# Optimization experiments

Hardware: AMD Instinct MI355X
Metric: run time of the kernel (lower is better)

The kernel has to match this reference:

```python
import jax, jax.numpy as jnp
import numpy as np

KS = 3      # kernel_size
PAD = 1     # padding
STRIDE = 1
B, C_IN, C_OUT, H, W = 4, 64, 128, 128, 128


def _conv(x, w, stride, padding):
    return jax.lax.conv_general_dilated(
        x, w, (stride, stride), padding,
        dimension_numbers=("NCHW", "OIHW", "NCHW"))


def setup_inputs() -> dict:
    key = jax.random.key(0)
    k1, k2, k3, k4 = jax.random.split(key, 4)
    N = KS * KS
    x = jax.random.normal(k1, (B, C_IN, H, W), jnp.float32)
    # offset conv: Conv2d(inc, 2*ks*ks, 3, padding=1, stride=1). (Original inits
    # weight to 0; we use small random weights so the bilinear gather is exercised.)
    w_off = jax.random.normal(k2, (2 * N, C_IN, 3, 3), jnp.float32) * 0.01
    b_off = jax.random.normal(k3, (2 * N,), jnp.float32) * 0.01
    # main conv: Conv2d(inc, outc, ks, stride=ks, bias=False)
    w_conv = jax.random.normal(k4, (C_OUT, C_IN, KS, KS), jnp.float32) / np.sqrt(C_IN * KS * KS)
    return {"x": x, "w_off": w_off, "b_off": b_off, "w_conv": w_conv}


def deform_forward(x, w_off, b_off, w_conv):
    ks, pad, stride = KS, PAD, STRIDE
    N = ks * ks
    offset = _conv(x, w_off, stride, [(1, 1), (1, 1)]) + b_off[None, :, None, None]
    b, _, h, w = offset.shape
    xp = jnp.pad(x, ((0, 0), (0, 0), (pad, pad), (pad, pad)))
    Hp, Wp = xp.shape[2], xp.shape[3]

    # p_n: relative kernel offsets, layout [y coords (N), x coords (N)]
    r = jnp.arange(-(ks - 1) // 2, (ks - 1) // 2 + 1)
    pny, pnx = jnp.meshgrid(r, r, indexing="ij")
    p_n = jnp.concatenate([pny.ravel(), pnx.ravel()]).astype(offset.dtype).reshape(1, 2 * N, 1, 1)

    # p_0: absolute output-pixel centers (1-based due to zero padding)
    p0y, p0x = jnp.meshgrid(jnp.arange(1, h * stride + 1, stride),
                            jnp.arange(1, w * stride + 1, stride), indexing="ij")
    p_0 = jnp.concatenate([jnp.tile(p0y[None, None], (1, N, 1, 1)),
                           jnp.tile(p0x[None, None], (1, N, 1, 1))], axis=1).astype(offset.dtype)

    p = (p_0 + p_n + offset).transpose(0, 2, 3, 1)  # (b, h, w, 2N)

    # four integer corners (indices are non-differentiable / detached)
    q_lt_f = jnp.floor(jax.lax.stop_gradient(p))
    q_rb_f = q_lt_f + 1

    def clamp_yx(q):
        return jnp.concatenate([jnp.clip(q[..., :N], 0, Hp - 1),
                                jnp.clip(q[..., N:], 0, Wp - 1)], axis=-1).astype(jnp.int32)

    q_lt = clamp_yx(q_lt_f)
    q_rb = clamp_yx(q_rb_f)
    q_lb = jnp.concatenate([q_lt[..., :N], q_rb[..., N:]], axis=-1)
    q_rt = jnp.concatenate([q_rb[..., :N], q_lt[..., N:]], axis=-1)

    # points falling in the padding region snap to floor(p)
    mask = jnp.concatenate([
        (p[..., :N] < pad) | (p[..., :N] > Hp - 1 - pad),
        (p[..., N:] < pad) | (p[..., N:] > Wp - 1 - pad)], axis=-1).astype(p.dtype)
    mask = jax.lax.stop_gradient(mask)
    floor_p = jnp.floor(p)
    p = p * (1 - mask) + floor_p * mask
    p = jnp.concatenate([jnp.clip(p[..., :N], 0, Hp - 1),
                         jnp.clip(p[..., N:], 0, Wp - 1)], axis=-1)

    f = lambda q: q.astype(p.dtype)
    g_lt = (1 + (f(q_lt[..., :N]) - p[..., :N])) * (1 + (f(q_lt[..., N:]) - p[..., N:]))
    g_rb = (1 - (f(q_rb[..., :N]) - p[..., :N])) * (1 - (f(q_rb[..., N:]) - p[..., N:]))
    g_lb = (1 + (f(q_lb[..., :N]) - p[..., :N])) * (1 - (f(q_lb[..., N:]) - p[..., N:]))
    g_rt = (1 - (f(q_rt[..., :N]) - p[..., :N])) * (1 + (f(q_rt[..., N:]) - p[..., N:]))

    c = xp.shape[1]
    x_flat = xp.reshape(b, c, Hp * Wp)  # (b, c, Hp*Wp)

    def get_x_q(q):
        idx = (q[..., :N] * Wp + q[..., N:]).reshape(b, 1, h * w * N)
        return jnp.take_along_axis(x_flat, idx, axis=2).reshape(b, c, h, w, N)

    x_off = (g_lt[:, None] * get_x_q(q_lt) + g_rb[:, None] * get_x_q(q_rb)
             + g_lb[:, None] * get_x_q(q_lb) + g_rt[:, None] * get_x_q(q_rt))

    # (b, c, h, w, N=ks*ks) -> (b, c, h*ks, w*ks): sample n maps to kernel cell (n//ks, n%ks)
    x_off = x_off.reshape(b, c, h, w, ks, ks).transpose(0, 1, 2, 4, 3, 5).reshape(b, c, h * ks, w * ks)

    return _conv(x_off, w_conv, ks, "VALID")  # stride=ks, no bias


def reference(x, w_off, b_off, w_conv):
    return deform_forward(x, w_off, b_off, w_conv)
```

## Files before the change

kernel.cpp:

```cpp
#include <hip/hip_runtime.h>
#include <hip/hip_fp16.h>

#define NB 4
#define CI 64
#define CO 128
#define HH 128
#define WW 128
#define HWSZ (HH*WW)
#define TOTPX (NB*HWSZ)
#define NN 9

using half8 = __attribute__((ext_vector_type(8))) _Float16;
using f32x4 = __attribute__((ext_vector_type(4))) float;
using f32x2 = __attribute__((ext_vector_type(2))) float;

__global__ __launch_bounds__(256) void k_prep_w(const float* __restrict__ w,
                                                unsigned short* __restrict__ waF,
                                                const float* __restrict__ w_off,
                                                float* __restrict__ wP) {
    int t = blockIdx.x * 256 + threadIdx.x;
    if (t < CO * 576) {
        int oc = t / 576, r = t - oc * 576;
        int c = r / 9, n = r - c * 9;
        int i = oc >> 4, col = oc & 15;
        int ks = c >> 5, koct = (c >> 3) & 3, e = c & 7;
        int lane = koct * 16 + col;
        waF[(n * 16 + i * 2 + ks) * 512 + lane * 8 + e] =
            __half_as_ushort(__float2half_rn(w[t]));
    }
    if (t < 18 * 576) {
        int oc = t / 576, r = t - oc * 576;
        wP[r * 20 + oc] = w_off[t];
    }
}

__global__ __launch_bounds__(512, 8) void k_offsets(
    const float* __restrict__ x, const float* __restrict__ wP,
    const float* __restrict__ b_off, uchar4* __restrict__ dC,
    ushort4* __restrict__ dG, unsigned short* __restrict__ xT)
{
    __shared__ f32x2 sm[512 * 9];
    int bid = blockIdx.x;
    int b = bid >> 8, rem = bid & 255, y = rem >> 1, x0 = (rem & 1) << 6;
    int t = threadIdx.x;
    int pxl = t & 63;
    int g   = __builtin_amdgcn_readfirstlane(t >> 6);
    int xg = x0 + pxl;

    f32x2 a2[9];
    #pragma unroll
    for (int i = 0; i < 9; i++) a2[i] = {0.f, 0.f};

    #pragma unroll 2
    for (int ci = 0; ci < 8; ci++) {
        int cg = g * 8 + ci;
        const float* xpl = x + (size_t)(b * CI + cg) * HWSZ;
        #pragma unroll
        for (int ky = 0; ky < 3; ky++) {
            int yy = y + ky - 1;
            if ((unsigned)yy >= 128u) continue;
            const float* xr = xpl + yy * WW;
            #pragma unroll
            for (int kx = 0; kx < 3; kx++) {
                int xx = xg + kx - 1;
                float v = ((unsigned)xx < 128u) ? xr[xx] : 0.f;
                const f32x2* wr2 = (const f32x2*)(wP + (cg * 9 + ky * 3 + kx) * 20);
                f32x2 v2 = {v, v};
                #pragma unroll
                for (int j = 0; j < 9; j++)
                    a2[j] = __builtin_elementwise_fma(v2, wr2[j], a2[j]);
            }
        }
    }

    {
        const float* xc = x + ((size_t)(b * CI + g * 8) * HH + y) * WW + xg;
        unsigned short c8[8];
        #pragma unroll
        for (int ci = 0; ci < 8; ci++)
            c8[ci] = __half_as_ushort(__float2half_rn(xc[(size_t)ci * HWSZ]));
        size_t pbase = (size_t)((b * HH + y) * WW + xg) * 64 + g * 8;
        *(uint4*)(xT + pbase) = *(const uint4*)&c8[0];
    }

    #pragma unroll
    for (int i = 0; i < 9; i++) sm[t * 9 + i] = a2[i];
    __syncthreads();

    for (int task = t; task < 576; task += 512) {
        int p2 = task & 63, n = task >> 6;
        float ay = b_off[n], ax = b_off[9 + n];
        int jy = n >> 1, cy = n & 1;
        int jx = (9 + n) >> 1, cx = (9 + n) & 1;
        #pragma unroll
        for (int gg = 0; gg < 8; gg++) {
            ay += sm[(gg * 64 + p2) * 9 + jy][cy];
            ax += sm[(gg * 64 + p2) * 9 + jx][cx];
        }
        float py  = (float)(y + (n / 3)) + ay;
        float pxc = (float)(x0 + p2 + (n % 3)) + ax;
        float fy = floorf(py), fx = floorf(pxc);
        if (py  < 1.f || py  > 128.f) py  = fy;
        if (pxc < 1.f || pxc > 128.f) pxc = fx;
        py  = fminf(fmaxf(py,  0.f), 129.f);
        pxc = fminf(fmaxf(pxc, 0.f), 129.f);

        fy = floorf(py); fx = floorf(pxc);
        int y0 = (int)fy, x0i = (int)fx;
        int y1 = min(y0 + 1, 129), x1 = min(x0i + 1, 129);
        float wyl = 1.f + (fy - py);
        float wyr = 1.f - ((float)y1 - py);
        float wxl = 1.f + (fx - pxc);
        float wxr = 1.f - ((float)x1 - pxc);
        float glt = wyl * wxl, grb = wyr * wxr, glb = wyl * wxr, grt = wyr * wxl;
        if ((unsigned)(y0  - 1) >= 128u) { glt = 0.f; glb = 0.f; }
        if ((unsigned)(y1  - 1) >= 128u) { grb = 0.f; grt = 0.f; }
        if ((unsigned)(x0i - 1) >= 128u) { glt = 0.f; grt = 0.f; }
        if ((unsigned)(x1  - 1) >= 128u) { grb = 0.f; glb = 0.f; }

        uchar4 cu;
        cu.x = (unsigned char)min(max(y0  - 1, 0), 127);
        cu.y = (unsigned char)min(max(y1  - 1, 0), 127);
        cu.z = (unsigned char)min(max(x0i - 1, 0), 127);
        cu.w = (unsigned char)min(max(x1  - 1, 0), 127);
        ushort4 gu;
        gu.x = __half_as_ushort(__float2half_rn(glt));
        gu.y = __half_as_ushort(__float2half_rn(grb));
        gu.z = __half_as_ushort(__float2half_rn(glb));
        gu.w = __half_as_ushort(__float2half_rn(grt));
        int pixIdx = (b * HH + y) * WW + x0 + p2;
        dC[n * TOTPX + pixIdx] = cu;
        dG[n * TOTPX + pixIdx] = gu;
    }
}

__global__ __launch_bounds__(256, 2) void k_main(
    const unsigned short* __restrict__ xT, const unsigned short* __restrict__ waF,
    const uchar4* __restrict__ dC, const ushort4* __restrict__ dG,
    float* __restrict__ out)
{
    __shared__ __align__(16) unsigned short Wl[2][8192];
    __shared__ __align__(16) unsigned short Rd[4][2][1024];

    int bid0 = blockIdx.x;
    int bid  = ((bid0 & 7) << 6) | (bid0 >> 3);
    int b = bid >> 7, y = bid & 127;

    int t = threadIdx.x, lane = t & 63, wv = t >> 6;
    int col = lane & 15, koct = lane >> 4;
    int gp = lane >> 2, gq = lane & 3;
    int qo = gq * 8;
    int rowbase = (b * HH + y) * WW;
    int pixG0 = rowbase + wv * 32 + gp;
    int pixG1 = pixG0 + 16;
    const unsigned short* xb = xT + (size_t)b * (HWSZ * 64);

    half8 raw0[8], raw1[8];
    f32x4 acc0[8], acc1[8];
    #pragma unroll
    for (int i = 0; i < 8; i++) { acc0[i] = {0.f,0.f,0.f,0.f}; acc1[i] = {0.f,0.f,0.f,0.f}; }

    auto stage = [&](int kc, int buf) {
        #pragma unroll
        for (int p = 0; p < 4; p++) {
            const unsigned short* gsrc = waF + kc * 8192 + wv * 512 + p * 2048 + lane * 8;
            __builtin_amdgcn_global_load_lds(
                (const __attribute__((address_space(1))) unsigned int*)gsrc,
                (__attribute__((address_space(3))) unsigned int*)&Wl[buf][wv * 512 + p * 2048],
                16, 0, 0);
        }
    };
    auto issue = [&](uchar4 cu, half8* raw) {
        int o00 = (((int)cu.x * WW) + (int)cu.z) << 6;
        int o11 = (((int)cu.y * WW) + (int)cu.w) << 6;
        int o01 = (((int)cu.x * WW) + (int)cu.w) << 6;
        int o10 = (((int)cu.y * WW) + (int)cu.z) << 6;
        raw[0] = *(const half8*)(xb + o00 + qo);
        raw[1] = *(const half8*)(xb + o11 + qo);
        raw[2] = *(const half8*)(xb + o01 + qo);
        raw[3] = *(const half8*)(xb + o10 + qo);
        raw[4] = *(const half8*)(xb + o00 + qo + 32);
        raw[5] = *(const half8*)(xb + o11 + qo + 32);
        raw[6] = *(const half8*)(xb + o01 + qo + 32);
        raw[7] = *(const half8*)(xb + o10 + qo + 32);
    };
    auto combine_store = [&](const half8* raw, ushort4 gu, unsigned short* rbase) {
        __half2 q0 = __half2half2(__ushort_as_half(gu.x));
        __half2 q1 = __half2half2(__ushort_as_half(gu.y));
        __half2 q2 = __half2half2(__ushort_as_half(gu.z));
        __half2 q3 = __half2half2(__ushort_as_half(gu.w));
        #pragma unroll
        for (int ks = 0; ks < 2; ks++) {
            __half2 vm[4];
            #pragma unroll
            for (int m = 0; m < 4; m++) {
                __half2 v = __hmul2(((const __half2*)&raw[ks * 4 + 0])[m], q0);
                v = __hfma2(((const __half2*)&raw[ks * 4 + 1])[m], q1, v);
                v = __hfma2(((const __half2*)&raw[ks * 4 + 2])[m], q2, v);
                v = __hfma2(((const __half2*)&raw[ks * 4 + 3])[m], q3, v);
                vm[m] = v;
            }
            int gz = (4 * ks + gq) ^ (gp & 7);
            *(uint4*)(rbase + gp * 64 + gz * 8) = *(const uint4*)vm;
        }
    };

    stage(0, 0);
    __builtin_amdgcn_sched_barrier(0);
    uchar4 cuA0 = dC[pixG0],         cuA1 = dC[pixG1];
    ushort4 guA0 = dG[pixG0],        guA1 = dG[pixG1];
    uchar4 cuB0 = dC[TOTPX + pixG0], cuB1 = dC[TOTPX + pixG1];
    ushort4 guB0 = dG[TOTPX + pixG0], guB1 = dG[TOTPX + pixG1];
    __builtin_amdgcn_sched_barrier(0);
    issue(cuA0, raw0);
    issue(cuA1, raw1);
    __builtin_amdgcn_sched_barrier(0);
    asm volatile("s_waitcnt vmcnt(24)" ::: "memory");
    __builtin_amdgcn_s_barrier();
    __builtin_amdgcn_sched_barrier(0);

#define ITER(KC)                                                              \
  {                                                                           \
    if ((KC) < 8) stage((KC) + 1, ((KC) & 1) ^ 1);                            \
    __builtin_amdgcn_sched_barrier(0);                                        \
    uchar4 cuN0, cuN1; ushort4 guN0, guN1;                                    \
    if ((KC) < 7) {                                                           \
      cuN0 = dC[((KC)+2) * TOTPX + pixG0]; guN0 = dG[((KC)+2) * TOTPX + pixG0]; \
      cuN1 = dC[((KC)+2) * TOTPX + pixG1]; guN1 = dG[((KC)+2) * TOTPX + pixG1]; \
    }                                                                         \
    __builtin_amdgcn_sched_barrier(0);                                        \
    combine_store(raw0, guA0, &Rd[wv][0][0]);                                 \
    combine_store(raw1, guA1, &Rd[wv][1][0]);                                 \
    asm volatile("s_waitcnt lgkmcnt(0)" ::: "memory");                        \
    __builtin_amdgcn_sched_barrier(0);                                        \
    half8 bfr0[2], bfr1[2];                                                   \
    _Pragma("unroll")                                                         \
    for (int ks = 0; ks < 2; ks++) {                                          \
      int gz = (4 * ks + koct) ^ (col & 7);                                   \
      bfr0[ks] = *(const half8*)(&Rd[wv][0][0] + col * 64 + gz * 8);          \
      bfr1[ks] = *(const half8*)(&Rd[wv][1][0] + col * 64 + gz * 8);          \
    }                                                                         \
    __builtin_amdgcn_sched_barrier(0);                                        \
    if ((KC) < 8) { issue(cuB0, raw0); issue(cuB1, raw1); }                   \
    __builtin_amdgcn_sched_barrier(0);                                        \
    __builtin_amdgcn_s_setprio(1);                                            \
    { const unsigned short* wl = &Wl[(KC) & 1][0];                            \
      _Pragma("unroll")                                                       \
      for (int ks = 0; ks < 2; ks++)                                          \
        _Pragma("unroll")                                                     \
        for (int i = 0; i < 8; i++) {                                         \
          half8 af = *(const half8*)(wl + (i * 2 + ks) * 512 + lane * 8);     \
          acc0[i] = __builtin_amdgcn_mfma_f32_16x16x32_f16(af, bfr0[ks],      \
                                                           acc0[i], 0, 0, 0); \
          acc1[i] = __builtin_amdgcn_mfma_f32_16x16x32_f16(af, bfr1[ks],      \
                                                           acc1[i], 0, 0, 0); \
        } }                                                                   \
    __builtin_amdgcn_s_setprio(0);                                            \
    if ((KC) < 8) {                                                           \
      if ((KC) < 7) asm volatile("s_waitcnt vmcnt(20)" ::: "memory");         \
      else          asm volatile("s_waitcnt vmcnt(16)" ::: "memory");         \
      __builtin_amdgcn_s_barrier();                                           \
      __builtin_amdgcn_sched_barrier(0);                                      \
    }                                                                         \
    guA0 = guB0; guA1 = guB1;                                                 \
    cuB0 = ((KC) < 7) ? cuN0 : cuB0; guB0 = ((KC) < 7) ? guN0 : guB0;         \
    cuB1 = ((KC) < 7) ? cuN1 : cuB1; guB1 = ((KC) < 7) ? guN1 : guB1;         \
  }

    ITER(0) ITER(1) ITER(2) ITER(3) ITER(4) ITER(5) ITER(6) ITER(7) ITER(8)
#undef ITER

    int ob0 = b * CO * HWSZ + y * WW + wv * 32 + col;
    #pragma unroll
    for (int i = 0; i < 8; i++)
        #pragma unroll
        for (int r = 0; r < 4; r++) {
            int oc = i * 16 + koct * 4 + r;
            out[ob0 + oc * HWSZ]      = acc0[i][r];
            out[ob0 + oc * HWSZ + 16] = acc1[i][r];
        }
}

extern "C" void kernel_launch(void* const* d_in, const int* in_sizes, int n_in,
                              void* d_out, int out_size, void* d_ws, size_t ws_size,
                              hipStream_t stream) {
    const float* x      = (const float*)d_in[0];
    const float* w_off  = (const float*)d_in[1];
    const float* b_off  = (const float*)d_in[2];
    const float* w_conv = (const float*)d_in[3];
    float* out = (float*)d_out;

    char* wsb = (char*)d_ws;
    unsigned short* xT  = (unsigned short*)wsb;
    uchar4*         dC  = (uchar4*)(wsb + (size_t)TOTPX * 64 * 2);
    ushort4*        dG  = (ushort4*)(wsb + (size_t)TOTPX * 64 * 2 + (size_t)NN * TOTPX * 4);
    unsigned short* waF = (unsigned short*)(wsb + (size_t)TOTPX * 64 * 2
                                            + (size_t)NN * TOTPX * 4 + (size_t)NN * TOTPX * 8);
    float*          wP  = (float*)(wsb + (size_t)TOTPX * 64 * 2
                                   + (size_t)NN * TOTPX * 4 + (size_t)NN * TOTPX * 8
                                   + (size_t)CO * 576 * 2);

    k_prep_w<<<(CO * 576 + 255) / 256, 256, 0, stream>>>(w_conv, waF, w_off, wP);
    k_offsets<<<1024, 512, 0, stream>>>(x, wP, b_off, dC, dG, xT);
    k_main<<<512, 256, 0, stream>>>(xT, waF, dC, dG, out);
}
```

Baseline: 57.39 us.

## Halve per-block pixel tile in k_main to raise occupancy and block count

```diff
diff --git a/kernel.cpp b/kernel.cpp
--- a/kernel.cpp
+++ b/kernel.cpp
@@ -134,31 +134,29 @@
     }
 }
 
-__global__ __launch_bounds__(256, 2) void k_main(
+__global__ __launch_bounds__(256, 4) void k_main(
     const unsigned short* __restrict__ xT, const unsigned short* __restrict__ waF,
     const uchar4* __restrict__ dC, const ushort4* __restrict__ dG,
     float* __restrict__ out)
 {
     __shared__ __align__(16) unsigned short Wl[2][8192];
-    __shared__ __align__(16) unsigned short Rd[4][2][1024];
+    __shared__ __align__(16) unsigned short Rd[4][1024];
 
     int bid0 = blockIdx.x;
-    int bid  = ((bid0 & 7) << 6) | (bid0 >> 3);
-    int b = bid >> 7, y = bid & 127;
+    int bid  = ((bid0 & 7) << 7) | (bid0 >> 3);
+    int b = bid >> 8, rem = bid & 255, y = rem >> 1, x0 = (rem & 1) << 6;
 
     int t = threadIdx.x, lane = t & 63, wv = t >> 6;
     int col = lane & 15, koct = lane >> 4;
     int gp = lane >> 2, gq = lane & 3;
     int qo = gq * 8;
-    int rowbase = (b * HH + y) * WW;
-    int pixG0 = rowbase + wv * 32 + gp;
-    int pixG1 = pixG0 + 16;
+    int pixG = (b * HH + y) * WW + x0 + wv * 16 + gp;
     const unsigned short* xb = xT + (size_t)b * (HWSZ * 64);
 
-    half8 raw0[8], raw1[8];
-    f32x4 acc0[8], acc1[8];
-    #pragma unroll
-    for (int i = 0; i < 8; i++) { acc0[i] = {0.f,0.f,0.f,0.f}; acc1[i] = {0.f,0.f,0.f,0.f}; }
+    half8 raw[8];
+    f32x4 acc[8];
+    #pragma unroll
+    for (int i = 0; i < 8; i++) acc[i] = {0.f, 0.f, 0.f, 0.f};
 
     auto stage = [&](int kc, int buf) {
         #pragma unroll
@@ -170,7 +168,7 @@
                 16, 0, 0);
         }
     };
-    auto issue = [&](uchar4 cu, half8* raw) {
+    auto issue = [&](uchar4 cu) {
         int o00 = (((int)cu.x * WW) + (int)cu.z) << 6;
         int o11 = (((int)cu.y * WW) + (int)cu.w) << 6;
         int o01 = (((int)cu.x * WW) + (int)cu.w) << 6;
@@ -184,7 +182,7 @@
         raw[6] = *(const half8*)(xb + o01 + qo + 32);
         raw[7] = *(const half8*)(xb + o10 + qo + 32);
     };
-    auto combine_store = [&](const half8* raw, ushort4 gu, unsigned short* rbase) {
+    auto combine_store = [&](ushort4 gu) {
         __half2 q0 = __half2half2(__ushort_as_half(gu.x));
         __half2 q1 = __half2half2(__ushort_as_half(gu.y));
         __half2 q2 = __half2half2(__ushort_as_half(gu.z));
@@ -201,21 +199,18 @@
                 vm[m] = v;
             }
             int gz = (4 * ks + gq) ^ (gp & 7);
-            *(uint4*)(rbase + gp * 64 + gz * 8) = *(const uint4*)vm;
+            *(uint4*)(&Rd[wv][0] + gp * 64 + gz * 8) = *(const uint4*)vm;
         }
     };
 
     stage(0, 0);
     __builtin_amdgcn_sched_barrier(0);
-    uchar4 cuA0 = dC[pixG0],         cuA1 = dC[pixG1];
-    ushort4 guA0 = dG[pixG0],        guA1 = dG[pixG1];
-    uchar4 cuB0 = dC[TOTPX + pixG0], cuB1 = dC[TOTPX + pixG1];
-    ushort4 guB0 = dG[TOTPX + pixG0], guB1 = dG[TOTPX + pixG1];
-    __builtin_amdgcn_sched_barrier(0);
-    issue(cuA0, raw0);
-    issue(cuA1, raw1);
-    __builtin_amdgcn_sched_barrier(0);
-    asm volatile("s_waitcnt vmcnt(24)" ::: "memory");
+    uchar4  cuA = dC[pixG];          ushort4 guA = dG[pixG];
+    uchar4  cuB = dC[TOTPX + pixG];  ushort4 guB = dG[TOTPX + pixG];
+    __builtin_amdgcn_sched_barrier(0);
+    issue(cuA);
+    __builtin_amdgcn_sched_barrier(0);
+    asm volatile("s_waitcnt vmcnt(8)" ::: "memory");
     __builtin_amdgcn_s_barrier();
     __builtin_amdgcn_sched_barrier(0);
 
@@ -223,25 +218,21 @@
   {                                                                           \
     if ((KC) < 8) stage((KC) + 1, ((KC) & 1) ^ 1);                            \
     __builtin_amdgcn_sched_barrier(0);                                        \
-    uchar4 cuN0, cuN1; ushort4 guN0, guN1;                                    \
-    if ((KC) < 7) {                                                           \
-      cuN0 = dC[((KC)+2) * TOTPX + pixG0]; guN0 = dG[((KC)+2) * TOTPX + pixG0]; \
-      cuN1 = dC[((KC)+2) * TOTPX + pixG1]; guN1 = dG[((KC)+2) * TOTPX + pixG1]; \
-    }                                                                         \
-    __builtin_amdgcn_sched_barrier(0);                                        \
-    combine_store(raw0, guA0, &Rd[wv][0][0]);                                 \
-    combine_store(raw1, guA1, &Rd[wv][1][0]);                                 \
+    uchar4 cuN; ushort4 guN;                                                  \
+    if ((KC) < 7) { cuN = dC[((KC)+2) * TOTPX + pixG];                        \
+                    guN = dG[((KC)+2) * TOTPX + pixG]; }                      \
+    __builtin_amdgcn_sched_barrier(0);                                        \
+    combine_store(guA);                                                       \
     asm volatile("s_waitcnt lgkmcnt(0)" ::: "memory");                        \
     __builtin_amdgcn_sched_barrier(0);                                        \
-    half8 bfr0[2], bfr1[2];                                                   \
+    half8 bfr[2];                                                             \
     _Pragma("unroll")                                                         \
     for (int ks = 0; ks < 2; ks++) {                                          \
       int gz = (4 * ks + koct) ^ (col & 7);                                   \
-      bfr0[ks] = *(const half8*)(&Rd[wv][0][0] + col * 64 + gz * 8);          \
-      bfr1[ks] = *(const half8*)(&Rd[wv][1][0] + col * 64 + gz * 8);          \
+      bfr[ks] = *(const half8*)(&Rd[wv][0] + col * 64 + gz * 8);              \
     }                                                                         \
     __builtin_amdgcn_sched_barrier(0);                                        \
-    if ((KC) < 8) { issue(cuB0, raw0); issue(cuB1, raw1); }                   \
+    if ((KC) < 8) issue(cuB);                                                 \
     __builtin_amdgcn_sched_barrier(0);                                        \
     __builtin_amdgcn_s_setprio(1);                                            \
     { const unsigned short* wl = &Wl[(KC) & 1][0];                            \
@@ -250,34 +241,29 @@
         _Pragma("unroll")                                                     \
         for (int i = 0; i < 8; i++) {                                         \
           half8 af = *(const half8*)(wl + (i * 2 + ks) * 512 + lane * 8);     \
-          acc0[i] = __builtin_amdgcn_mfma_f32_16x16x32_f16(af, bfr0[ks],      \
-                                                           acc0[i], 0, 0, 0); \
-          acc1[i] = __builtin_amdgcn_mfma_f32_16x16x32_f16(af, bfr1[ks],      \
-                                                           acc1[i], 0, 0, 0); \
-        } }                                                                   \
+          acc[i] = __builtin_amdgcn_mfma_f32_16x16x32_f16(af, bfr[ks],        \
+                                                          acc[i], 0, 0, 0); } } \
     __builtin_amdgcn_s_setprio(0);                                            \
     if ((KC) < 8) {                                                           \
-      if ((KC) < 7) asm volatile("s_waitcnt vmcnt(20)" ::: "memory");         \
-      else          asm volatile("s_waitcnt vmcnt(16)" ::: "memory");         \
+      if ((KC) < 7) asm volatile("s_waitcnt vmcnt(10)" ::: "memory");         \
+      else          asm volatile("s_waitcnt vmcnt(8)"  ::: "memory");         \
       __builtin_amdgcn_s_barrier();                                           \
       __builtin_amdgcn_sched_barrier(0);                                      \
     }                                                                         \
-    guA0 = guB0; guA1 = guB1;                                                 \
-    cuB0 = ((KC) < 7) ? cuN0 : cuB0; guB0 = ((KC) < 7) ? guN0 : guB0;         \
-    cuB1 = ((KC) < 7) ? cuN1 : cuB1; guB1 = ((KC) < 7) ? guN1 : guB1;         \
+    cuA = cuB; guA = guB;                                                     \
+    cuB = ((KC) < 7) ? cuN : cuB; guB = ((KC) < 7) ? guN : guB;               \
   }
 
     ITER(0) ITER(1) ITER(2) ITER(3) ITER(4) ITER(5) ITER(6) ITER(7) ITER(8)
 #undef ITER
 
-    int ob0 = b * CO * HWSZ + y * WW + wv * 32 + col;
+    int ob0 = b * CO * HWSZ + y * WW + x0 + wv * 16 + col;
     #pragma unroll
     for (int i = 0; i < 8; i++)
         #pragma unroll
         for (int r = 0; r < 4; r++) {
             int oc = i * 16 + koct * 4 + r;
-            out[ob0 + oc * HWSZ]      = acc0[i][r];
-            out[ob0 + oc * HWSZ + 16] = acc1[i][r];
+            out[ob0 + oc * HWSZ] = acc[i][r];
         }
 }
 
@@ -302,5 +288,5 @@
 
     k_prep_w<<<(CO * 576 + 255) / 256, 256, 0, stream>>>(w_conv, waF, w_off, wP);
     k_offsets<<<1024, 512, 0, stream>>>(x, wP, b_off, dC, dG, xT);
-    k_main<<<512, 256, 0, stream>>>(xT, waF, dC, dG, out);
-}
+    k_main<<<1024, 256, 0, stream>>>(xT, waF, dC, dG, out);
+}
```

Result: no change. 58.39 us (+1.7%).

## Compute two adjacent pixels per thread in offset conv with float2 loads

Applied to the files above, without the earlier changes.

```diff
diff --git a/kernel.cpp b/kernel.cpp
--- a/kernel.cpp
+++ b/kernel.cpp
@@ -34,24 +34,24 @@
     }
 }
 
-__global__ __launch_bounds__(512, 8) void k_offsets(
+__global__ __launch_bounds__(512, 4) void k_offsets(
     const float* __restrict__ x, const float* __restrict__ wP,
     const float* __restrict__ b_off, uchar4* __restrict__ dC,
     ushort4* __restrict__ dG, unsigned short* __restrict__ xT)
 {
-    __shared__ f32x2 sm[512 * 9];
+    __shared__ f32x2 sm[4 * 128 * 9];
     int bid = blockIdx.x;
-    int b = bid >> 8, rem = bid & 255, y = rem >> 1, x0 = (rem & 1) << 6;
+    int b = bid >> 7, y = bid & 127;
     int t = threadIdx.x;
-    int pxl = t & 63;
-    int g   = __builtin_amdgcn_readfirstlane(t >> 6);
-    int xg = x0 + pxl;
-
-    f32x2 a2[9];
-    #pragma unroll
-    for (int i = 0; i < 9; i++) a2[i] = {0.f, 0.f};
-
-    #pragma unroll 2
+    int pr = t & 63;
+    int g  = __builtin_amdgcn_readfirstlane(t >> 6);
+
+    f32x2 a0[9], a1[9];
+    #pragma unroll
+    for (int i = 0; i < 9; i++) { a0[i] = {0.f, 0.f}; a1[i] = {0.f, 0.f}; }
+    unsigned short c16a[8], c16b[8];
+
+    #pragma unroll
     for (int ci = 0; ci < 8; ci++) {
         int cg = g * 8 + ci;
         const float* xpl = x + (size_t)(b * CI + cg) * HWSZ;
@@ -59,78 +59,117 @@
         for (int ky = 0; ky < 3; ky++) {
             int yy = y + ky - 1;
             if ((unsigned)yy >= 128u) continue;
-            const float* xr = xpl + yy * WW;
+            const float* xr = xpl + yy * WW + 2 * pr;
+            int offL = (pr > 0)  ? -2 : 0;
+            int offR = (pr < 63) ?  2 : 0;
+            f32x2 v0 = *(const f32x2*)(xr);
+            f32x2 vl = *(const f32x2*)(xr + offL);
+            f32x2 vr = *(const f32x2*)(xr + offR);
+            if (pr == 0)  vl = (f32x2){0.f, 0.f};
+            if (pr == 63) vr = (f32x2){0.f, 0.f};
+            if (ky == 1) {
+                c16a[ci] = __half_as_ushort(__float2half_rn(v0[0]));
+                c16b[ci] = __half_as_ushort(__float2half_rn(v0[1]));
+            }
             #pragma unroll
             for (int kx = 0; kx < 3; kx++) {
-                int xx = xg + kx - 1;
-                float v = ((unsigned)xx < 128u) ? xr[xx] : 0.f;
+                float ta = (kx == 0) ? vl[1] : (kx == 1) ? v0[0] : v0[1];
+                float tb = (kx == 0) ? v0[0] : (kx == 1) ? v0[1] : vr[0];
                 const f32x2* wr2 = (const f32x2*)(wP + (cg * 9 + ky * 3 + kx) * 20);
-                f32x2 v2 = {v, v};
+                f32x2 va = {ta, ta}, vb = {tb, tb};
                 #pragma unroll
-                for (int j = 0; j < 9; j++)
-                    a2[j] = __builtin_elementwise_fma(v2, wr2[j], a2[j]);
+                for (int j = 0; j < 9; j++) {
+                    a0[j] = __builtin_elementwise_fma(va, wr2[j], a0[j]);
+                    a1[j] = __builtin_elementwise_fma(vb, wr2[j], a1[j]);
+                }
             }
         }
     }
 
     {
-        const float* xc = x + ((size_t)(b * CI + g * 8) * HH + y) * WW + xg;
-        unsigned short c8[8];
-        #pragma unroll
-        for (int ci = 0; ci < 8; ci++)
-            c8[ci] = __half_as_ushort(__float2half_rn(xc[(size_t)ci * HWSZ]));
-        size_t pbase = (size_t)((b * HH + y) * WW + xg) * 64 + g * 8;
-        *(uint4*)(xT + pbase) = *(const uint4*)&c8[0];
-    }
-
-    #pragma unroll
-    for (int i = 0; i < 9; i++) sm[t * 9 + i] = a2[i];
+        size_t p0 = (size_t)((b * HH + y) * WW + 2 * pr) * 64 + g * 8;
+        *(uint4*)(xT + p0)      = *(const uint4*)&c16a[0];
+        *(uint4*)(xT + p0 + 64) = *(const uint4*)&c16b[0];
+    }
+
+    if (g < 4) {
+        int base0 = (g * 128 + 2 * pr) * 9;
+        #pragma unroll
+        for (int j = 0; j < 9; j++) { sm[base0 + j] = a0[j]; sm[base0 + 9 + j] = a1[j]; }
+    }
     __syncthreads();
-
-    for (int task = t; task < 576; task += 512) {
-        int p2 = task & 63, n = task >> 6;
-        float ay = b_off[n], ax = b_off[9 + n];
-        int jy = n >> 1, cy = n & 1;
-        int jx = (9 + n) >> 1, cx = (9 + n) & 1;
-        #pragma unroll
-        for (int gg = 0; gg < 8; gg++) {
-            ay += sm[(gg * 64 + p2) * 9 + jy][cy];
-            ax += sm[(gg * 64 + p2) * 9 + jx][cx];
-        }
-        float py  = (float)(y + (n / 3)) + ay;
-        float pxc = (float)(x0 + p2 + (n % 3)) + ax;
-        float fy = floorf(py), fx = floorf(pxc);
-        if (py  < 1.f || py  > 128.f) py  = fy;
-        if (pxc < 1.f || pxc > 128.f) pxc = fx;
-        py  = fminf(fmaxf(py,  0.f), 129.f);
-        pxc = fminf(fmaxf(pxc, 0.f), 129.f);
-
-        fy = floorf(py); fx = floorf(pxc);
-        int y0 = (int)fy, x0i = (int)fx;
-        int y1 = min(y0 + 1, 129), x1 = min(x0i + 1, 129);
-        float wyl = 1.f + (fy - py);
-        float wyr = 1.f - ((float)y1 - py);
-        float wxl = 1.f + (fx - pxc);
-        float wxr = 1.f - ((float)x1 - pxc);
-        float glt = wyl * wxl, grb = wyr * wxr, glb = wyl * wxr, grt = wyr * wxl;
-        if ((unsigned)(y0  - 1) >= 128u) { glt = 0.f; glb = 0.f; }
-        if ((unsigned)(y1  - 1) >= 128u) { grb = 0.f; grt = 0.f; }
-        if ((unsigned)(x0i - 1) >= 128u) { glt = 0.f; grt = 0.f; }
-        if ((unsigned)(x1  - 1) >= 128u) { grb = 0.f; glb = 0.f; }
-
-        uchar4 cu;
-        cu.x = (unsigned char)min(max(y0  - 1, 0), 127);
-        cu.y = (unsigned char)min(max(y1  - 1, 0), 127);
-        cu.z = (unsigned char)min(max(x0i - 1, 0), 127);
-        cu.w = (unsigned char)min(max(x1  - 1, 0), 127);
-        ushort4 gu;
-        gu.x = __half_as_ushort(__float2half_rn(glt));
-        gu.y = __half_as_ushort(__float2half_rn(grb));
-        gu.z = __half_as_ushort(__float2half_rn(glb));
-        gu.w = __half_as_ushort(__float2half_rn(grt));
-        int pixIdx = (b * HH + y) * WW + x0 + p2;
-        dC[n * TOTPX + pixIdx] = cu;
-        dG[n * TOTPX + pixIdx] = gu;
+    float ay[3], ax[3];
+    #pragma unroll
+    for (int it = 0; it < 3; it++) {
+        int task = t + it * 512;
+        if (task < 1152) {
+            int p2 = task & 127, n = task >> 7;
+            float sy = b_off[n], sx = b_off[9 + n];
+            int jy = n >> 1, cy = n & 1;
+            int jx = (9 + n) >> 1, cx = (9 + n) & 1;
+            #pragma unroll
+            for (int gg = 0; gg < 4; gg++) {
+                sy += sm[(gg * 128 + p2) * 9 + jy][cy];
+                sx += sm[(gg * 128 + p2) * 9 + jx][cx];
+            }
+            ay[it] = sy; ax[it] = sx;
+        } else { ay[it] = 0.f; ax[it] = 0.f; }
+    }
+    __syncthreads();
+    if (g >= 4) {
+        int base0 = ((g - 4) * 128 + 2 * pr) * 9;
+        #pragma unroll
+        for (int j = 0; j < 9; j++) { sm[base0 + j] = a0[j]; sm[base0 + 9 + j] = a1[j]; }
+    }
+    __syncthreads();
+    #pragma unroll
+    for (int it = 0; it < 3; it++) {
+        int task = t + it * 512;
+        if (task < 1152) {
+            int p2 = task & 127, n = task >> 7;
+            float sy = ay[it], sx = ax[it];
+            int jy = n >> 1, cy = n & 1;
+            int jx = (9 + n) >> 1, cx = (9 + n) & 1;
+            #pragma unroll
+            for (int gg = 0; gg < 4; gg++) {
+                sy += sm[(gg * 128 + p2) * 9 + jy][cy];
+                sx += sm[(gg * 128 + p2) * 9 + jx][cx];
+            }
+            float py  = (float)(y + (n / 3)) + sy;
+            float pxc = (float)(p2 + (n % 3)) + sx;
+            float fy = floorf(py), fx = floorf(pxc);
+            if (py  < 1.f || py  > 128.f) py  = fy;
+            if (pxc < 1.f || pxc > 128.f) pxc = fx;
+            py  = fminf(fmaxf(py,  0.f), 129.f);
+            pxc = fminf(fmaxf(pxc, 0.f), 129.f);
+
+            fy = floorf(py); fx = floorf(pxc);
+            int y0 = (int)fy, x0i = (int)fx;
+            int y1 = min(y0 + 1, 129), x1 = min(x0i + 1, 129);
+            float wyl = 1.f + (fy - py);
+            float wyr = 1.f - ((float)y1 - py);
+            float wxl = 1.f + (fx - pxc);
+            float wxr = 1.f - ((float)x1 - pxc);
+            float glt = wyl * wxl, grb = wyr * wxr, glb = wyl * wxr, grt = wyr * wxl;
+            if ((unsigned)(y0  - 1) >= 128u) { glt = 0.f; glb = 0.f; }
+            if ((unsigned)(y1  - 1) >= 128u) { grb = 0.f; grt = 0.f; }
+            if ((unsigned)(x0i - 1) >= 128u) { glt = 0.f; grt = 0.f; }
+            if ((unsigned)(x1  - 1) >= 128u) { grb = 0.f; glb = 0.f; }
+
+            uchar4 cu;
+            cu.x = (unsigned char)min(max(y0  - 1, 0), 127);
+            cu.y = (unsigned char)min(max(y1  - 1, 0), 127);
+            cu.z = (unsigned char)min(max(x0i - 1, 0), 127);
+            cu.w = (unsigned char)min(max(x1  - 1, 0), 127);
+            ushort4 gu;
+            gu.x = __half_as_ushort(__float2half_rn(glt));
+            gu.y = __half_as_ushort(__float2half_rn(grb));
+            gu.z = __half_as_ushort(__float2half_rn(glb));
+            gu.w = __half_as_ushort(__float2half_rn(grt));
+            int pixIdx = (b * HH + y) * WW + p2;
+            dC[n * TOTPX + pixIdx] = cu;
+            dG[n * TOTPX + pixIdx] = gu;
+        }
     }
 }
 
@@ -215,7 +254,7 @@
     issue(cuA0, raw0);
     issue(cuA1, raw1);
     __builtin_amdgcn_sched_barrier(0);
-    asm volatile("s_waitcnt vmcnt(24)" ::: "memory");
+    asm volatile("s_waitcnt vmcnt(16)" ::: "memory");
     __builtin_amdgcn_s_barrier();
     __builtin_amdgcn_sched_barrier(0);
 
@@ -301,6 +340,6 @@
                                    + (size_t)CO * 576 * 2);
 
     k_prep_w<<<(CO * 576 + 255) / 256, 256, 0, stream>>>(w_conv, waF, w_off, wP);
-    k_offsets<<<1024, 512, 0, stream>>>(x, wP, b_off, dC, dG, xT);
+    k_offsets<<<512, 512, 0, stream>>>(x, wP, b_off, dC, dG, xT);
     k_main<<<512, 256, 0, stream>>>(xT, waF, dC, dG, out);
 }
```

Result: faster. 55.00 us (median of 2 runs) (-4.2%).
